# Kernel optimization log

Hardware: AMD Instinct MI355X
Metric: run time of the kernel (lower is better)

The kernel has to match this reference:

```python
import jax, jax.numpy as jnp
import numpy as np

B, S, D, H, HD, MLP = 2, 4096, 512, 8, 64, 2048
BLK, C = 128, 32  # Fixed1Pattern(block_size=128), Fixed2Pattern(block_size=128, c=32)
EPS = 1e-6


def _xavier(key, shape, fan_in, fan_out):
    lim = np.sqrt(6.0 / (fan_in + fan_out)).astype(np.float32)
    return jax.random.uniform(key, shape, jnp.float32, -lim, lim)


def setup_inputs() -> dict:
    key = jax.random.key(0)
    ks = jax.random.split(key, 9)
    return {
        "inputs": jax.random.normal(ks[0], (B, S, D), jnp.float32),
        "ln1_scale": jnp.ones((D,), jnp.float32),
        "ln1_bias": jnp.zeros((D,), jnp.float32),
        "wq": _xavier(ks[1], (D, H, HD), D, H * HD),
        "wk": _xavier(ks[2], (D, H, HD), D, H * HD),
        "wv": _xavier(ks[3], (D, H, HD), D, H * HD),
        "wo": _xavier(ks[4], (H, HD, D), H * HD, D),
        "ln2_scale": jnp.ones((D,), jnp.float32),
        "ln2_bias": jnp.zeros((D,), jnp.float32),
        "w1": _xavier(ks[5], (D, MLP), D, MLP),
        "b1": jax.random.normal(ks[6], (MLP,), jnp.float32) * 1e-6,
        "w2": _xavier(ks[7], (MLP, D), MLP, D),
        "b2": jax.random.normal(ks[8], (D,), jnp.float32) * 1e-6,
    }


def _layer_norm(x, scale, bias):
    mu = jnp.mean(x, axis=-1, keepdims=True)
    var = jnp.mean(jnp.square(x - mu), axis=-1, keepdims=True)
    return (x - mu) * jax.lax.rsqrt(var + EPS) * scale + bias


def _sparse_mask():
    # Union of causal Fixed1 (same block) and Fixed2 (last C columns of each block) patterns.
    i = jnp.arange(S)[:, None]
    j = jnp.arange(S)[None, :]
    causal = j <= i
    local = (i // BLK) == (j // BLK)            # Fixed1: within-block
    strided = (j % BLK) >= (BLK - C)            # Fixed2: block-summary columns
    return causal & (local | strided)           # [S, S] bool


def reference(inputs, ln1_scale, ln1_bias, wq, wk, wv, wo,
              ln2_scale, ln2_bias, w1, b1, w2, b2):
    x = _layer_norm(inputs, ln1_scale, ln1_bias)
    q = jnp.einsum("bsd,dhk->bshk", x, wq)
    k = jnp.einsum("bsd,dhk->bshk", x, wk)
    v = jnp.einsum("bsd,dhk->bshk", x, wv)
    scale = 1.0 / np.sqrt(HD).astype(np.float32)
    scores = jnp.einsum("bqhk,bshk->bhqs", q * scale, k)  # [B,H,S,S]
    mask = _sparse_mask()[None, None]
    scores = jnp.where(mask, scores, jnp.float32(-1e9))
    attn = jax.nn.softmax(scores, axis=-1)
    ctx = jnp.einsum("bhqs,bshk->bqhk", attn, v)
    attn_out = jnp.einsum("bqhk,hkd->bqd", ctx, wo)
    x = attn_out + inputs  # residual 1 (dropout deterministic)
    y = _layer_norm(x, ln2_scale, ln2_bias)
    y = jax.nn.gelu(y @ w1 + b1) @ w2 + b2  # MlpBlock
    return x + y
```

## Files before the change

### kernel.cpp

```cpp
#include <hip/hip_runtime.h>
#include <hip/hip_bf16.h>

typedef __attribute__((ext_vector_type(8))) __bf16 bf16x8;
typedef __attribute__((ext_vector_type(8))) short s16x8;
typedef __attribute__((ext_vector_type(4))) float f32x4;

#define NB 2
#define NS 4096
#define ND 512
#define NH 8
#define NHD 64
#define NMLP 2048

__device__ __forceinline__ unsigned short f2b(float f) {
  __hip_bfloat16 h = __float2bfloat16(f);
  return __builtin_bit_cast(unsigned short, h);
}

__device__ __forceinline__ float geluf(float x) {
  float u = 0.7978845608028654f * (x + 0.044715f * x * x * x);
  return x / (1.0f + __expf(-2.0f * u));
}

__device__ __forceinline__ void gload16(const void* g, void* l) {
  __builtin_amdgcn_global_load_lds((const __attribute__((address_space(1))) void*)g,
                                   (__attribute__((address_space(3))) void*)l, 16, 0, 0);
}

__global__ __launch_bounds__(256) void prep_weights(const float* __restrict__ wq,
                                                    const float* __restrict__ wk,
                                                    const float* __restrict__ wv,
                                                    const float* __restrict__ wo,
                                                    const float* __restrict__ w1,
                                                    const float* __restrict__ w2,
                                                    unsigned short* __restrict__ qkvT,
                                                    unsigned short* __restrict__ woT,
                                                    unsigned short* __restrict__ w1T,
                                                    unsigned short* __restrict__ w2T) {
  __shared__ unsigned short lt[64][66];
  const int tile = blockIdx.x, t = threadIdx.x;
  const float* src;
  unsigned short* dst;
  int R, C, tr, tc;
  float sc = 1.0f;
  if (tile < 256) {
    int seg = tile >> 6, tt = tile & 63;
    R = 512; C = 512;
    src = seg == 0 ? wq : seg == 1 ? wk : seg == 2 ? wv : wo;
    dst = (seg < 3) ? (qkvT + ((size_t)seg << 18)) : woT;
    if (seg == 0) sc = 0.125f;
    tr = tt >> 3; tc = tt & 7;
  } else if (tile < 512) {
    int tt = tile - 256;
    R = 512; C = 2048; src = w1; dst = w1T;
    tr = tt >> 5; tc = tt & 31;
  } else {
    int tt = tile - 512;
    R = 2048; C = 512; src = w2; dst = w2T;
    tr = tt >> 3; tc = tt & 7;
  }
  const int r0 = tr * 64, c0 = tc * 64;
  const int fx = t & 15, fy = t >> 4;
#pragma unroll
  for (int p = 0; p < 4; ++p) {
    int rr = p * 16 + fy;
    float4 v = *(const float4*)&src[(size_t)(r0 + rr) * C + c0 + fx * 4];
    lt[rr][fx * 4 + 0] = f2b(v.x * sc);
    lt[rr][fx * 4 + 1] = f2b(v.y * sc);
    lt[rr][fx * 4 + 2] = f2b(v.z * sc);
    lt[rr][fx * 4 + 3] = f2b(v.w * sc);
  }
  __syncthreads();
#pragma unroll
  for (int p = 0; p < 4; ++p) {
    int cc = p * 16 + fy;
    ushort4 o;
    o.x = lt[fx * 4 + 0][cc];
    o.y = lt[fx * 4 + 1][cc];
    o.z = lt[fx * 4 + 2][cc];
    o.w = lt[fx * 4 + 3][cc];
    *(ushort4*)&dst[(size_t)(c0 + cc) * R + r0 + fx * 4] = o;
  }
}

__global__ __launch_bounds__(256) void ln_bf16(const float* __restrict__ x,
                                               const float* __restrict__ g,
                                               const float* __restrict__ bta,
                                               unsigned short* __restrict__ out) {
  const int t = threadIdx.x, l = t & 63, w = t >> 6;
  const size_t row = (size_t)blockIdx.x * 4 + w;
  const float4* xr = (const float4*)(x + row * ND);
  float4 a = xr[l];
  float4 bq = xr[64 + l];
  float s = a.x + a.y + a.z + a.w + bq.x + bq.y + bq.z + bq.w;
  float ss = a.x * a.x + a.y * a.y + a.z * a.z + a.w * a.w +
             bq.x * bq.x + bq.y * bq.y + bq.z * bq.z + bq.w * bq.w;
#pragma unroll
  for (int msk = 1; msk <= 32; msk <<= 1) {
    s += __shfl_xor(s, msk);
    ss += __shfl_xor(ss, msk);
  }
  float mu = s * (1.0f / ND);
  float var = ss * (1.0f / ND) - mu * mu;
  float rr = rsqrtf(var + 1e-6f);
  const float4* g4 = (const float4*)g;
  const float4* b4 = (const float4*)bta;
  float4 g0 = g4[l], g1 = g4[64 + l], b0 = b4[l], b1 = b4[64 + l];
  ushort4 o0, o1;
  o0.x = f2b((a.x - mu) * rr * g0.x + b0.x);
  o0.y = f2b((a.y - mu) * rr * g0.y + b0.y);
  o0.z = f2b((a.z - mu) * rr * g0.z + b0.z);
  o0.w = f2b((a.w - mu) * rr * g0.w + b0.w);
  o1.x = f2b((bq.x - mu) * rr * g1.x + b1.x);
  o1.y = f2b((bq.y - mu) * rr * g1.y + b1.y);
  o1.z = f2b((bq.z - mu) * rr * g1.z + b1.z);
  o1.w = f2b((bq.w - mu) * rr * g1.w + b1.w);
  ushort4* orow = (ushort4*)(out + row * ND);
  orow[l] = o0;
  orow[64 + l] = o1;
}

template <int EPI>
__global__ __launch_bounds__(512) void gemm_bt(const unsigned short* __restrict__ A,
                                               const unsigned short* __restrict__ Bt,
                                               int M, int N, int K,
                                               unsigned short* __restrict__ ob,
                                               float* __restrict__ of,
                                               const float* __restrict__ addf,
                                               const float* __restrict__ bias) {
  __shared__ unsigned short lA[2][128 * 64];
  __shared__ unsigned short lB[2][128 * 64];
  const int t = threadIdx.x;
  const int l = t & 63, w = t >> 6;
  const int wr = w >> 2, wc = w & 3;
  const int gx = gridDim.x;
  const int nwg = gx * gridDim.y;
  const int fid = blockIdx.y * gx + blockIdx.x;
  const int q8 = nwg >> 3, r8 = nwg & 7, xcd = fid & 7, idx = fid >> 3;
  const int lid = (xcd < r8 ? xcd * (q8 + 1) : r8 * (q8 + 1) + (xcd - r8) * q8) + idx;
  const int bm = lid / gx, bn = lid % gx;
  const size_t rowBytes = (size_t)K * 2;
  const char* Ab = (const char*)A + (size_t)bm * 128 * rowBytes;
  const char* Bb = (const char*)Bt + (size_t)bn * 128 * rowBytes;
  const int sr0 = t >> 3;
  const int scb = (((t & 7) ^ ((t >> 3) & 7)) << 4);
  f32x4 acc[4][2] = {};

  auto stage = [&](int buf, int k0) {
    char* dA = (char*)&lA[buf][0] + t * 16;
    char* dB = (char*)&lB[buf][0] + t * 16;
#pragma unroll
    for (int i = 0; i < 2; ++i) {
      const size_t go = (size_t)(sr0 + i * 64) * rowBytes + 2 * k0 + scb;
      gload16(Ab + go, dA + i * 8192);
      gload16(Bb + go, dB + i * 8192);
    }
  };

  const int nkt = K >> 6;
  stage(0, 0);
  int cur = 0;
  for (int kt = 0; kt < nkt; ++kt) {
    if (kt + 1 < nkt) {
      stage(cur ^ 1, (kt + 1) * 64);
      asm volatile("s_waitcnt vmcnt(4)" ::: "memory");
    } else {
      asm volatile("s_waitcnt vmcnt(0)" ::: "memory");
    }
    __builtin_amdgcn_s_barrier();
    __builtin_amdgcn_sched_barrier(0);
#pragma unroll
    for (int ks = 0; ks < 2; ++ks) {
      const int xg = ((ks * 4 + (l >> 4)) ^ (l & 7)) * 8;
      bf16x8 aF[4], bF[2];
#pragma unroll
      for (int m = 0; m < 4; ++m)
        aF[m] = *(const bf16x8*)&lA[cur][(wr * 64 + m * 16 + (l & 15)) * 64 + xg];
#pragma unroll
      for (int n = 0; n < 2; ++n)
        bF[n] = *(const bf16x8*)&lB[cur][(wc * 32 + n * 16 + (l & 15)) * 64 + xg];
      __builtin_amdgcn_s_setprio(1);
#pragma unroll
      for (int m = 0; m < 4; ++m)
#pragma unroll
        for (int n = 0; n < 2; ++n)
          acc[m][n] = __builtin_amdgcn_mfma_f32_16x16x32_bf16(aF[m], bF[n], acc[m][n], 0, 0, 0);
      __builtin_amdgcn_s_setprio(0);
    }
    asm volatile("s_waitcnt lgkmcnt(0)" ::: "memory");
    __builtin_amdgcn_s_barrier();
    cur ^= 1;
  }
#pragma unroll
  for (int m = 0; m < 4; ++m)
#pragma unroll
    for (int n = 0; n < 2; ++n) {
      int row0 = bm * 128 + wr * 64 + m * 16 + (l >> 4) * 4;
      int col = bn * 128 + wc * 32 + n * 16 + (l & 15);
      if constexpr (EPI == 0) {
        int part = col >> 9, nn = col & 511;
        int hh = nn >> 6, hd = nn & 63;
        int b = row0 >> 12, sidx0 = row0 & 4095;
        if (part < 2) {
#pragma unroll
          for (int j = 0; j < 4; ++j)
            ob[((((size_t)part * NB + b) * NH + hh) * NS + sidx0 + j) * NHD + hd] =
                f2b(acc[m][n][j]);
        } else {
          ushort4 o;
          o.x = f2b(acc[m][n][0]);
          o.y = f2b(acc[m][n][1]);
          o.z = f2b(acc[m][n][2]);
          o.w = f2b(acc[m][n][3]);
          *(ushort4*)&ob[(size_t)2 * NB * NH * NS * NHD +
                         (((size_t)b * NH + hh) * NHD + hd) * NS + sidx0] = o;
        }
      } else if constexpr (EPI == 2) {
#pragma unroll
        for (int j = 0; j < 4; ++j) {
          size_t i = (size_t)(row0 + j) * NMLP + col;
          ob[i] = f2b(geluf(acc[m][n][j] + bias[col]));
        }
      } else {
#pragma unroll
        for (int j = 0; j < 4; ++j) {
          int row = row0 + j;
          float v = acc[m][n][j];
          if constexpr (EPI == 1) {
            size_t i = (size_t)row * ND + col;
            of[i] = v + addf[i];
          } else {
            size_t i = (size_t)row * ND + col;
            of[i] = v + bias[col] + addf[i];
          }
        }
      }
    }
}

__global__ __launch_bounds__(512, 4) void attn_sparse(const unsigned short* __restrict__ qm,
                                                      const unsigned short* __restrict__ km,
                                                      const unsigned short* __restrict__ vTg,
                                                      unsigned short* __restrict__ ctx) {
  __shared__ unsigned short kl[2][128 * 64];
  __shared__ unsigned short vt[2][64 * 128];
  __shared__ unsigned short pl[8][16 * 64];
  const int t = threadIdx.x, l = t & 63, w = t >> 6;
  const int bid = blockIdx.x;
  const int hh = bid & 7;
  const int jj = bid >> 3;
  const int b = jj >> 5;
  const int qb = (jj < 32) ? jj : 63 - jj;
  const size_t bh = ((size_t)b * NH + hh) * NS;
  const size_t bhd = ((size_t)b * NH + hh) * NHD;
  const int qrow0 = qb * 128 + w * 16;
  bf16x8 qa[2];
#pragma unroll
  for (int ks = 0; ks < 2; ++ks)
    qa[ks] = *(const bf16x8*)&qm[(bh + qrow0 + (l & 15)) * NHD + ks * 32 + (l >> 4) * 8];
  f32x4 c[4] = {};
  float mrun[4], lrun[4];
#pragma unroll
  for (int j = 0; j < 4; ++j) { mrun[j] = -1e30f; lrun[j] = 0.0f; }

  const int nsum128 = qb >> 2, rem = qb & 3;
  const int nSumCh = nsum128 + (rem ? 1 : 0);
  const int nch = nSumCh + 1;

  const int kr_ = t >> 3;
  const int ku_ = (t & 7) ^ (kr_ & 7);
  const int vr_ = t >> 4;
  const int vu_ = ((t & 15) & 8) | (((t & 15) & 7) ^ (vr_ & 7));

  auto keyOf = [&](int c2, int kk) -> int {
    return (c2 < nSumCh) ? ((c2 * 4 + (kk >> 5)) * 128 + 96 + (kk & 31)) : (qb * 128 + kk);
  };
  auto stage = [&](int buf, int c2) {
    const int krow0 = keyOf(c2, kr_);
    gload16(&km[(bh + krow0) * NHD + ku_ * 8], (char*)&kl[buf][0] + t * 16);
    const int krow1 = keyOf(c2, kr_ + 64);
    gload16(&km[(bh + krow1) * NHD + ku_ * 8], (char*)&kl[buf][0] + 8192 + t * 16);
    const int gk = keyOf(c2, vu_ * 8);
    gload16(&vTg[(bhd + vr_) * NS + gk], (char*)&vt[buf][0] + t * 16);
    gload16(&vTg[(bhd + vr_ + 32) * NS + gk], (char*)&vt[buf][0] + 8192 + t * 16);
  };

  const int e_ = l & 7, q_ = l >> 4;
  const int kx0 = (q_ ^ e_) * 8;
  const int kx1 = ((4 + q_) ^ e_) * 8;
  const int r4_ = (q_ & 1) << 2;

  stage(0, 0);
  int cur = 0;
  for (int ch = 0; ch < nch; ++ch) {
    if (ch + 1 < nch) {
      stage(cur ^ 1, ch + 1);
      asm volatile("s_waitcnt vmcnt(4)" ::: "memory");
    } else {
      asm volatile("s_waitcnt vmcnt(0)" ::: "memory");
    }
    __builtin_amdgcn_s_barrier();
    __builtin_amdgcn_sched_barrier(0);

    const bool isLocal = (ch == nch - 1);
    const bool isRem = (rem != 0) && !isLocal && (ch == nsum128);
    const int nT = isLocal ? (w + 1) : (isRem ? 2 * rem : 8);
    const int nTpl = isLocal ? ((w | 1) + 1) : nT;
    const int nKs = nTpl >> 1;

    f32x4 sf[8];
#pragma unroll
    for (int n = 0; n < 8; ++n) {
      if (n < nT) {
        const int row = n * 16 + (l & 15);
        const bf16x8 k0 = *(const bf16x8*)&kl[cur][row * 64 + kx0];
        const bf16x8 k1 = *(const bf16x8*)&kl[cur][row * 64 + kx1];
        f32x4 a = {};
        a = __builtin_amdgcn_mfma_f32_16x16x32_bf16(qa[0], k0, a, 0, 0, 0);
        a = __builtin_amdgcn_mfma_f32_16x16x32_bf16(qa[1], k1, a, 0, 0, 0);
        if (isLocal && n == w) {
#pragma unroll
          for (int j = 0; j < 4; ++j)
            if ((l & 15) > q_ * 4 + j) a[j] = -1e9f;
        }
        sf[n] = a;
      }
    }
    float cm[4];
#pragma unroll
    for (int j = 0; j < 4; ++j) cm[j] = -1e30f;
#pragma unroll
    for (int n = 0; n < 8; ++n)
      if (n < nT)
#pragma unroll
        for (int j = 0; j < 4; ++j) cm[j] = fmaxf(cm[j], sf[n][j]);
#pragma unroll
    for (int j = 0; j < 4; ++j) {
      cm[j] = fmaxf(cm[j], __shfl_xor(cm[j], 1));
      cm[j] = fmaxf(cm[j], __shfl_xor(cm[j], 2));
      cm[j] = fmaxf(cm[j], __shfl_xor(cm[j], 4));
      cm[j] = fmaxf(cm[j], __shfl_xor(cm[j], 8));
    }
    bool need = false;
#pragma unroll
    for (int j = 0; j < 4; ++j) need |= (cm[j] > mrun[j] + 8.0f);
    if (__any(need)) {
      float al[4];
#pragma unroll
      for (int j = 0; j < 4; ++j) {
        float nm = fmaxf(mrun[j], cm[j]);
        al[j] = __expf(mrun[j] - nm);
        mrun[j] = nm;
      }
#pragma unroll
      for (int n = 0; n < 4; ++n)
#pragma unroll
        for (int j = 0; j < 4; ++j) c[n][j] *= al[j];
#pragma unroll
      for (int j = 0; j < 4; ++j) lrun[j] *= al[j];
    }
    float rs[4] = {0.f, 0.f, 0.f, 0.f};
#pragma unroll
    for (int n = 0; n < 8; ++n)
      if (n < nT)
#pragma unroll
        for (int j = 0; j < 4; ++j) {
          float p = __expf(sf[n][j] - mrun[j]);
          sf[n][j] = p;
          rs[j] += p;
        }
#pragma unroll
    for (int j = 0; j < 4; ++j) {
      rs[j] += __shfl_xor(rs[j], 1);
      rs[j] += __shfl_xor(rs[j], 2);
      rs[j] += __shfl_xor(rs[j], 4);
      rs[j] += __shfl_xor(rs[j], 8);
      lrun[j] += rs[j];
    }
#pragma unroll
    for (int h = 0; h < 2; ++h) {
      if (h * 4 < nTpl) {
#pragma unroll
        for (int n2 = 0; n2 < 4; ++n2) {
          const int n = h * 4 + n2;
          const int cu = n2 * 2 + ((l >> 3) & 1);
#pragma unroll
          for (int j = 0; j < 4; ++j) {
            if (n < nTpl) {
              unsigned short pv = 0;
              if (n < nT) pv = f2b(sf[n][j]);
              const int rowp = q_ * 4 + j;
              pl[w][rowp * 64 + (cu ^ (r4_ | j)) * 8 + e_] = pv;
            }
          }
        }
#pragma unroll
        for (int ks2 = 0; ks2 < 2; ++ks2) {
          const int ks = h * 2 + ks2;
          if (ks < nKs) {
            const bf16x8 pa =
                *(const bf16x8*)&pl[w][(l & 15) * 64 + (ks2 ? kx1 : kx0)];
#pragma unroll
            for (int nd = 0; nd < 4; ++nd) {
              const bf16x8 vb = *(const bf16x8*)&vt[cur][(nd * 16 + (l & 15)) * 128 +
                                                         ((ks & 2) << 5) +
                                                         (ks2 ? kx1 : kx0)];
              c[nd] = __builtin_amdgcn_mfma_f32_16x16x32_bf16(pa, vb, c[nd], 0, 0, 0);
            }
          }
        }
      }
    }
    __builtin_amdgcn_s_barrier();
    cur ^= 1;
  }
  float rinv[4];
#pragma unroll
  for (int j = 0; j < 4; ++j) rinv[j] = 1.0f / lrun[j];
#pragma unroll
  for (int n = 0; n < 4; ++n)
#pragma unroll
    for (int j = 0; j < 4; ++j) {
      int srow = qrow0 + q_ * 4 + j;
      int col = n * 16 + (l & 15);
      ctx[((size_t)b * NS + srow) * ND + hh * NHD + col] = f2b(c[n][j] * rinv[j]);
    }
}

extern "C" void kernel_launch(void* const* d_in, const int* in_sizes, int n_in,
                              void* d_out, int out_size, void* d_ws, size_t ws_size,
                              hipStream_t stream) {
  (void)in_sizes; (void)n_in; (void)out_size; (void)ws_size;
  const float* inputs = (const float*)d_in[0];
  const float* ln1s = (const float*)d_in[1];
  const float* ln1b = (const float*)d_in[2];
  const float* wq = (const float*)d_in[3];
  const float* wk = (const float*)d_in[4];
  const float* wv = (const float*)d_in[5];
  const float* wo = (const float*)d_in[6];
  const float* ln2s = (const float*)d_in[7];
  const float* ln2b = (const float*)d_in[8];
  const float* w1 = (const float*)d_in[9];
  const float* b1 = (const float*)d_in[10];
  const float* w2 = (const float*)d_in[11];
  const float* b2 = (const float*)d_in[12];
  float* out = (float*)d_out;

  unsigned short* xln = (unsigned short*)d_ws;
  unsigned short* xln2 = xln + (size_t)8192 * 512;
  unsigned short* ctx = xln2 + (size_t)8192 * 512;
  unsigned short* qkv = ctx + (size_t)8192 * 512;
  float* xres = (float*)(qkv + (size_t)3 * 8192 * 512);
  unsigned short* hbuf = (unsigned short*)(xres + (size_t)8192 * 512);
  unsigned short* qkvT = hbuf + (size_t)8192 * 2048;
  unsigned short* woT = qkvT + (size_t)1536 * 512;
  unsigned short* w1T = woT + (size_t)512 * 512;
  unsigned short* w2T = w1T + (size_t)2048 * 512;

  prep_weights<<<768, 256, 0, stream>>>(wq, wk, wv, wo, w1, w2, qkvT, woT, w1T, w2T);
  ln_bf16<<<2048, 256, 0, stream>>>(inputs, ln1s, ln1b, xln);
  gemm_bt<0><<<dim3(12, 64), 512, 0, stream>>>(xln, qkvT, 8192, 1536, 512,
                                               qkv, nullptr, nullptr, nullptr);
  attn_sparse<<<512, 512, 0, stream>>>(qkv, qkv + (size_t)8192 * 512,
                                       qkv + (size_t)2 * 8192 * 512, ctx);
  gemm_bt<1><<<dim3(4, 64), 512, 0, stream>>>(ctx, woT, 8192, 512, 512,
                                              nullptr, xres, inputs, nullptr);
  ln_bf16<<<2048, 256, 0, stream>>>(xres, ln2s, ln2b, xln2);
  gemm_bt<2><<<dim3(16, 64), 512, 0, stream>>>(xln2, w1T, 8192, 2048, 512,
                                               hbuf, nullptr, nullptr, b1);
  gemm_bt<3><<<dim3(4, 64), 512, 0, stream>>>(hbuf, w2T, 8192, 512, 2048,
                                              nullptr, out, xres, b2);
}
```

Measured before the change: 157.3 us.

## Split attention blocks into half-query-block workgroups and drop K/V double buffering

The sparse attention kernel now launches 1024 workgroups of 256 threads, each handling 64 query rows (half of a 128-row block), instead of 512 workgroups of 512 threads. Shared K/V staging becomes single-buffered, so each chunk is loaded and fully awaited before compute. The aim is more, smaller workgroups for better occupancy and load balance with less LDS per block. In exchange, K/V chunks are loaded twice (once per half), and load latency is no longer overlapped with compute.

```diff
diff --git a/kernel.cpp b/kernel.cpp
--- a/kernel.cpp
+++ b/kernel.cpp
@@ -238,22 +238,24 @@
     }
 }
 
-__global__ __launch_bounds__(512, 4) void attn_sparse(const unsigned short* __restrict__ qm,
-                                                      const unsigned short* __restrict__ km,
-                                                      const unsigned short* __restrict__ vTg,
-                                                      unsigned short* __restrict__ ctx) {
-  __shared__ unsigned short kl[2][128 * 64];
-  __shared__ unsigned short vt[2][64 * 128];
-  __shared__ unsigned short pl[8][16 * 64];
+__global__ __launch_bounds__(256) void attn_sparse(const unsigned short* __restrict__ qm,
+                                                   const unsigned short* __restrict__ km,
+                                                   const unsigned short* __restrict__ vTg,
+                                                   unsigned short* __restrict__ ctx) {
+  __shared__ unsigned short kl[128 * 64];
+  __shared__ unsigned short vt[64 * 128];
+  __shared__ unsigned short pl[4][16 * 64];
   const int t = threadIdx.x, l = t & 63, w = t >> 6;
   const int bid = blockIdx.x;
   const int hh = bid & 7;
-  const int jj = bid >> 3;
-  const int b = jj >> 5;
-  const int qb = (jj < 32) ? jj : 63 - jj;
+  const int u_ = bid >> 3;
+  const int k_ = u_ & 31, g_ = u_ >> 5;
+  const int b = g_ >> 1, hf = g_ & 1;
+  const int qb = hf ? (31 - k_) : k_;
+  const int wp = hf * 4 + w;
   const size_t bh = ((size_t)b * NH + hh) * NS;
   const size_t bhd = ((size_t)b * NH + hh) * NHD;
-  const int qrow0 = qb * 128 + w * 16;
+  const int qrow0 = qb * 128 + hf * 64 + w * 16;
   bf16x8 qa[2];
 #pragma unroll
   for (int ks = 0; ks < 2; ++ks)
@@ -267,22 +269,24 @@
   const int nSumCh = nsum128 + (rem ? 1 : 0);
   const int nch = nSumCh + 1;
 
-  const int kr_ = t >> 3;
-  const int ku_ = (t & 7) ^ (kr_ & 7);
-  const int vr_ = t >> 4;
-  const int vu_ = ((t & 15) & 8) | (((t & 15) & 7) ^ (vr_ & 7));
-
   auto keyOf = [&](int c2, int kk) -> int {
     return (c2 < nSumCh) ? ((c2 * 4 + (kk >> 5)) * 128 + 96 + (kk & 31)) : (qb * 128 + kk);
   };
-  auto stage = [&](int buf, int c2) {
-    const int krow0 = keyOf(c2, kr_);
-    gload16(&km[(bh + krow0) * NHD + ku_ * 8], (char*)&kl[buf][0] + t * 16);
-    const int krow1 = keyOf(c2, kr_ + 64);
-    gload16(&km[(bh + krow1) * NHD + ku_ * 8], (char*)&kl[buf][0] + 8192 + t * 16);
-    const int gk = keyOf(c2, vu_ * 8);
-    gload16(&vTg[(bhd + vr_) * NS + gk], (char*)&vt[buf][0] + t * 16);
-    gload16(&vTg[(bhd + vr_ + 32) * NS + gk], (char*)&vt[buf][0] + 8192 + t * 16);
+  auto stage = [&](int c2) {
+#pragma unroll
+    for (int i = 0; i < 4; ++i) {
+      const int flat = t + 256 * i;
+      const int rowk = flat >> 3, puk = flat & 7;
+      gload16(&km[(bh + keyOf(c2, rowk)) * NHD + (puk ^ (rowk & 7)) * 8],
+              (char*)kl + flat * 16);
+    }
+#pragma unroll
+    for (int i = 0; i < 4; ++i) {
+      const int flat = t + 256 * i;
+      const int rowv = flat >> 4, puv = flat & 15;
+      const int lu = (puv & 8) | ((puv & 7) ^ (rowv & 7));
+      gload16(&vTg[(bhd + rowv) * NS + keyOf(c2, lu * 8)], (char*)vt + flat * 16);
+    }
   };
 
   const int e_ = l & 7, q_ = l >> 4;
@@ -290,22 +294,16 @@
   const int kx1 = ((4 + q_) ^ e_) * 8;
   const int r4_ = (q_ & 1) << 2;
 
-  stage(0, 0);
-  int cur = 0;
   for (int ch = 0; ch < nch; ++ch) {
-    if (ch + 1 < nch) {
-      stage(cur ^ 1, ch + 1);
-      asm volatile("s_waitcnt vmcnt(4)" ::: "memory");
-    } else {
-      asm volatile("s_waitcnt vmcnt(0)" ::: "memory");
-    }
+    stage(ch);
+    asm volatile("s_waitcnt vmcnt(0)" ::: "memory");
     __builtin_amdgcn_s_barrier();
     __builtin_amdgcn_sched_barrier(0);
 
     const bool isLocal = (ch == nch - 1);
     const bool isRem = (rem != 0) && !isLocal && (ch == nsum128);
-    const int nT = isLocal ? (w + 1) : (isRem ? 2 * rem : 8);
-    const int nTpl = isLocal ? ((w | 1) + 1) : nT;
+    const int nT = isLocal ? (wp + 1) : (isRem ? 2 * rem : 8);
+    const int nTpl = isLocal ? ((wp | 1) + 1) : nT;
     const int nKs = nTpl >> 1;
 
     f32x4 sf[8];
@@ -313,12 +311,12 @@
     for (int n = 0; n < 8; ++n) {
       if (n < nT) {
         const int row = n * 16 + (l & 15);
-        const bf16x8 k0 = *(const bf16x8*)&kl[cur][row * 64 + kx0];
-        const bf16x8 k1 = *(const bf16x8*)&kl[cur][row * 64 + kx1];
+        const bf16x8 k0 = *(const bf16x8*)&kl[row * 64 + kx0];
+        const bf16x8 k1 = *(const bf16x8*)&kl[row * 64 + kx1];
         f32x4 a = {};
         a = __builtin_amdgcn_mfma_f32_16x16x32_bf16(qa[0], k0, a, 0, 0, 0);
         a = __builtin_amdgcn_mfma_f32_16x16x32_bf16(qa[1], k1, a, 0, 0, 0);
-        if (isLocal && n == w) {
+        if (isLocal && n == wp) {
 #pragma unroll
           for (int j = 0; j < 4; ++j)
             if ((l & 15) > q_ * 4 + j) a[j] = -1e9f;
@@ -402,9 +400,8 @@
                 *(const bf16x8*)&pl[w][(l & 15) * 64 + (ks2 ? kx1 : kx0)];
 #pragma unroll
             for (int nd = 0; nd < 4; ++nd) {
-              const bf16x8 vb = *(const bf16x8*)&vt[cur][(nd * 16 + (l & 15)) * 128 +
-                                                         ((ks & 2) << 5) +
-                                                         (ks2 ? kx1 : kx0)];
+              const bf16x8 vb = *(const bf16x8*)&vt[(nd * 16 + (l & 15)) * 128 +
+                                                    ((ks & 2) << 5) + (ks2 ? kx1 : kx0)];
               c[nd] = __builtin_amdgcn_mfma_f32_16x16x32_bf16(pa, vb, c[nd], 0, 0, 0);
             }
           }
@@ -412,7 +409,6 @@
       }
     }
     __builtin_amdgcn_s_barrier();
-    cur ^= 1;
   }
   float rinv[4];
 #pragma unroll
@@ -461,8 +457,8 @@
   ln_bf16<<<2048, 256, 0, stream>>>(inputs, ln1s, ln1b, xln);
   gemm_bt<0><<<dim3(12, 64), 512, 0, stream>>>(xln, qkvT, 8192, 1536, 512,
                                                qkv, nullptr, nullptr, nullptr);
-  attn_sparse<<<512, 512, 0, stream>>>(qkv, qkv + (size_t)8192 * 512,
-                                       qkv + (size_t)2 * 8192 * 512, ctx);
+  attn_sparse<<<1024, 256, 0, stream>>>(qkv, qkv + (size_t)8192 * 512,
+                                        qkv + (size_t)2 * 8192 * 512, ctx);
   gemm_bt<1><<<dim3(4, 64), 512, 0, stream>>>(ctx, woT, 8192, 512, 512,
                                               nullptr, xres, inputs, nullptr);
   ln_bf16<<<2048, 256, 0, stream>>>(xres, ln2s, ln2b, xln2);
```

Result: slower. 170.4 us (+8.3%).
